# Kernel tuning notes

Hardware: AMD Instinct MI355X
Metric: run time of the kernel (lower is better)

## Reference

```python
import jax, jax.numpy as jnp
import numpy as np
import math

HEAD_DIM = 32
N_Q_HEADS = 32
N_KV_HEADS = 8
ROPE_BASE = 10000.0
NEG_INF = -1e9


def _rope_cos_sin(seq_len, dtype):
    inv_freq = 1.0 / (ROPE_BASE ** (jnp.arange(0, HEAD_DIM, 2, dtype=jnp.float32) / HEAD_DIM))
    pos = jnp.arange(seq_len, dtype=jnp.float32)
    freqs = pos[:, None] * inv_freq[None, :]          # [S, D/2]
    emb = jnp.concatenate([freqs, freqs], axis=-1)     # [S, D]
    return jnp.cos(emb).astype(dtype), jnp.sin(emb).astype(dtype)


def _rotate_half(x):
    x1, x2 = jnp.split(x, 2, axis=-1)
    return jnp.concatenate([-x2, x1], axis=-1)


def _apply_rope(x, cos, sin):
    # x: [B, H, S, D]; cos/sin: [S, D]
    return x * cos[None, None] + _rotate_half(x) * sin[None, None]


def setup_inputs() -> dict:
    key = jax.random.key(0)
    ks = jax.random.split(key, 5)
    B, S, D = 2, 2048, 1024
    sc = 1.0 / math.sqrt(D)
    return {
        "hidden_states": jax.random.normal(ks[0], (B, S, D), jnp.float32),
        "attention_mask": jnp.ones((B, S), jnp.int32),
        "Wq": jax.random.normal(ks[1], (1024, 1024), jnp.float32) * sc,
        "Wk": jax.random.normal(ks[2], (256, 1024), jnp.float32) * sc,
        "Wv": jax.random.normal(ks[3], (256, 1024), jnp.float32) * sc,
        "Wo": jax.random.normal(ks[4], (1024, 1024), jnp.float32) * sc,
    }


def reference(hidden_states, attention_mask, Wq, Wk, Wv, Wo):
    B, S, D = hidden_states.shape
    group = N_Q_HEADS // N_KV_HEADS

    q = (hidden_states @ Wq.T).reshape(B, S, N_Q_HEADS, HEAD_DIM).transpose(0, 2, 1, 3)
    k = (hidden_states @ Wk.T).reshape(B, S, N_KV_HEADS, HEAD_DIM).transpose(0, 2, 1, 3)
    v = (hidden_states @ Wv.T).reshape(B, S, N_KV_HEADS, HEAD_DIM).transpose(0, 2, 1, 3)

    cos, sin = _rope_cos_sin(S, q.dtype)
    q = _apply_rope(q, cos, sin)
    k = _apply_rope(k, cos, sin)

    k = jnp.repeat(k, group, axis=1)  # [B, 32, S, D]
    v = jnp.repeat(v, group, axis=1)

    scores = jnp.einsum("bhqd,bhkd->bhqk", q, k) / math.sqrt(HEAD_DIM)

    causal = jnp.tril(jnp.ones((S, S), bool))
    allowed = causal[None, None] & (attention_mask[:, None, None, :] != 0)
    scores = jnp.where(allowed, scores, NEG_INF)

    attn = jax.nn.softmax(scores, axis=-1)
    out = jnp.einsum("bhqk,bhkd->bhqd", attn, v)  # [B, 32, S, 32]
    out = out.transpose(0, 2, 1, 3).reshape(B, S, D)
    return out @ Wo.T
```

## Files before the change

### kernel.cpp

```cpp
#include <hip/hip_runtime.h>

typedef __bf16 bf16x8 __attribute__((ext_vector_type(8)));
typedef __bf16 bf16x4 __attribute__((ext_vector_type(4)));
typedef float f32x4 __attribute__((ext_vector_type(4)));

__device__ __forceinline__ f32x4 mfma16(bf16x8 a, bf16x8 b, f32x4 c) {
  return __builtin_amdgcn_mfma_f32_16x16x32_bf16(a, b, c, 0, 0, 0);
}

__device__ __forceinline__ float fast_exp2(float x) {
  return __builtin_amdgcn_exp2f(x);
}

__global__ __launch_bounds__(256) void prep(const float* __restrict__ hidden,
                                            const float* __restrict__ Wq,
                                            const float* __restrict__ Wk,
                                            const float* __restrict__ Wv,
                                            const float* __restrict__ Wo,
                                            __bf16* __restrict__ hb,
                                            __bf16* __restrict__ Wqkvb,
                                            __bf16* __restrict__ Wob) {
  int q = blockIdx.x * 256 + threadIdx.x;
  const float* src;
  __bf16* dst;
  if (q < 1048576) {
    src = hidden; dst = hb;
  } else if ((q -= 1048576) < 262144) {
    src = Wq; dst = Wqkvb;
  } else if ((q -= 262144) < 65536) {
    src = Wk; dst = Wqkvb + 1048576;
  } else if ((q -= 65536) < 65536) {
    src = Wv; dst = Wqkvb + 1310720;
  } else {
    q -= 65536;
    src = Wo; dst = Wob;
  }
  float4 v = *(const float4*)(src + (size_t)q * 4);
  bf16x4 o = { (__bf16)v.x, (__bf16)v.y, (__bf16)v.z, (__bf16)v.w };
  *(bf16x4*)(dst + (size_t)q * 4) = o;
}

template <bool BF16_OUT>
__global__ __launch_bounds__(256) void gemm_nt(const __bf16* __restrict__ A,
                                               const __bf16* __restrict__ B,
                                               void* __restrict__ Cv, int N) {
  __shared__ __bf16 As[2][128][32];
  __shared__ __bf16 Bs[2][128][32];
  const int m0 = blockIdx.x * 128, n0 = blockIdx.y * 128;
  const int tid = threadIdx.x;
  const int wave = tid >> 6, lane = tid & 63, quad = lane >> 4, l16 = lane & 15;
  const int wr = wave >> 1, wc = wave & 1;
  const int sr = tid >> 1, sc = (tid & 1) * 16;
  f32x4 acc[4][4] = {};
  const __bf16* Ap = A + (size_t)(m0 + sr) * 1024 + sc;
  const __bf16* Bp = B + (size_t)(n0 + sr) * 1024 + sc;
  {
    uint4 a0 = *(const uint4*)Ap, a1 = *(const uint4*)(Ap + 8);
    uint4 b0 = *(const uint4*)Bp, b1 = *(const uint4*)(Bp + 8);
    *(uint4*)&As[0][sr][sc] = a0;
    *(uint4*)&As[0][sr][sc + 8] = a1;
    *(uint4*)&Bs[0][sr][sc] = b0;
    *(uint4*)&Bs[0][sr][sc + 8] = b1;
  }
  __syncthreads();
  int buf = 0;
  for (int k0 = 0; k0 < 1024; k0 += 32) {
    const bool more = (k0 + 32) < 1024;
    uint4 na0, na1, nb0, nb1;
    if (more) {
      na0 = *(const uint4*)(Ap + k0 + 32);
      na1 = *(const uint4*)(Ap + k0 + 40);
      nb0 = *(const uint4*)(Bp + k0 + 32);
      nb1 = *(const uint4*)(Bp + k0 + 40);
    }
    bf16x8 af[4], bfr[4];
#pragma unroll
    for (int i = 0; i < 4; i++)
      af[i] = *(bf16x8*)&As[buf][64 * wr + 16 * i + l16][quad * 8];
#pragma unroll
    for (int j = 0; j < 4; j++)
      bfr[j] = *(bf16x8*)&Bs[buf][64 * wc + 16 * j + l16][quad * 8];
#pragma unroll
    for (int i = 0; i < 4; i++)
#pragma unroll
      for (int j = 0; j < 4; j++) acc[i][j] = mfma16(af[i], bfr[j], acc[i][j]);
    if (more) {
      *(uint4*)&As[buf ^ 1][sr][sc] = na0;
      *(uint4*)&As[buf ^ 1][sr][sc + 8] = na1;
      *(uint4*)&Bs[buf ^ 1][sr][sc] = nb0;
      *(uint4*)&Bs[buf ^ 1][sr][sc + 8] = nb1;
    }
    __syncthreads();
    buf ^= 1;
  }
#pragma unroll
  for (int i = 0; i < 4; i++)
#pragma unroll
    for (int j = 0; j < 4; j++)
#pragma unroll
      for (int r = 0; r < 4; r++) {
        int row = m0 + 64 * wr + 16 * i + quad * 4 + r;
        int col = n0 + 64 * wc + 16 * j + l16;
        if constexpr (BF16_OUT)
          ((__bf16*)Cv)[(size_t)row * N + col] = (__bf16)acc[i][j][r];
        else
          ((float*)Cv)[(size_t)row * N + col] = acc[i][j][r];
      }
}

__global__ __launch_bounds__(256) void ropevt(__bf16* __restrict__ QKV,
                                              __bf16* __restrict__ VT,
                                              const int* __restrict__ amask,
                                              float* __restrict__ maskb) {
  int idx = blockIdx.x * 256 + threadIdx.x;
  if (idx < 2621440) {
    __bf16* base;
    int m, i;
    if (idx < 2097152) {
      m = idx >> 9;
      int h = (idx >> 4) & 31;
      i = idx & 15;
      base = QKV + (size_t)m * 1536 + h * 32;
    } else {
      int j = idx - 2097152;
      m = j >> 7;
      int h = (j >> 4) & 7;
      i = j & 15;
      base = QKV + (size_t)m * 1536 + 1024 + h * 32;
    }
    int s = m & 2047;
    float inv = __expf(-(float)i * 0.5756462732485114f);
    float ang = (float)s * inv;
    float sn, cs;
    __sincosf(ang, &sn, &cs);
    float x0 = (float)base[i];
    float x1 = (float)base[i + 16];
    base[i] = (__bf16)(x0 * cs - x1 * sn);
    base[i + 16] = (__bf16)(x1 * cs + x0 * sn);
  } else {
    int j = idx - 2621440;
    if (j < 4096) maskb[j] = amask[j] ? -16.0f : -1.5e9f;
    int s4 = j & 511;
    int d = (j >> 9) & 31;
    int hb_ = j >> 14;
    int s = s4 * 4;
    int b_ = hb_ >> 3, hkv_ = hb_ & 7;
    const __bf16* src = QKV + (size_t)(b_ * 2048 + s) * 1536 + 1280 + hkv_ * 32 + d;
    bf16x4 ov = { src[0], src[1536], src[3072], src[4608] };
    *(bf16x4*)&VT[((size_t)hb_ * 32 + d) * 2048 + s] = ov;
  }
}

__global__ __launch_bounds__(256, 4) void attn(const __bf16* __restrict__ QKV,
                                               const __bf16* __restrict__ VT,
                                               const float* __restrict__ maskb,
                                               __bf16* __restrict__ Ob) {
  __shared__ __bf16 Ks[2][64][40];
  __shared__ __bf16 Vs[2][32][72];
  __shared__ __bf16 Pl[4][2][16][72];
  const int tid = threadIdx.x;
  const int wave = tid >> 6, lane = tid & 63;
  const int quad = lane >> 4, l16 = lane & 15;
  const int b = blockIdx.z, h = blockIdx.y, hkv = h >> 2;
  const int xp = blockIdx.x;
  const float SC2 = 0.25503472f;

  const int sk_key = tid >> 2, sk_ch = (tid & 3) * 8;
  const int sv_d = tid >> 3, sv_seg = (tid & 7) * 8;
  const __bf16* ksrc = QKV + (size_t)(b * 2048 + sk_key) * 1536 + 1024 + hkv * 32 + sk_ch;
  const __bf16* vsrc = VT + ((size_t)(b * 8 + hkv) * 32 + sv_d) * 2048 + sv_seg;
  const float* mrow = maskb + b * 2048;

  for (int sp = 0; sp < 2; sp++) {
    const int strip = sp ? 15 - xp : xp;
    const int qw = strip * 128 + wave * 32;
    const int q_row0 = qw + l16, q_row1 = qw + 16 + l16;
    const __bf16* qbase = QKV + (size_t)(b * 2048 + qw + l16) * 1536 + h * 32 + quad * 8;
    bf16x8 qf0 = *(const bf16x8*)qbase;
    bf16x8 qf1 = *(const bf16x8*)(qbase + 16 * 1536);

    {
      uint4 kr = *(const uint4*)ksrc;
      uint4 vr = *(const uint4*)vsrc;
      *(uint4*)&Ks[0][sk_key][sk_ch] = kr;
      *(uint4*)&Vs[0][sv_d][sv_seg] = vr;
    }
    __syncthreads();

    f32x4 o00 = {}, o01 = {}, o10 = {}, o11 = {};
    float rs0 = 0.f, rs1 = 0.f;
    int buf = 0;
    const int ntiles = 2 * strip + 2;

    for (int t = 0; t < ntiles; t++) {
      const int kv0 = t << 6;
      const bool more = (t + 1 < ntiles);
      uint4 kr, vr;
      if (more) {
        kr = *(const uint4*)(ksrc + (size_t)(t + 1) * 64 * 1536);
        vr = *(const uint4*)(vsrc + (size_t)(t + 1) * 64);
      }
      if (kv0 <= qw + 31) {
        bf16x8 kf[4];
#pragma unroll
        for (int kt = 0; kt < 4; kt++)
          kf[kt] = *(bf16x8*)&Ks[buf][16 * kt + l16][quad * 8];
        f32x4 s0[4], s1[4];
#pragma unroll
        for (int kt = 0; kt < 4; kt++) {
          f32x4 z = {};
          s0[kt] = mfma16(kf[kt], qf0, z);
          s1[kt] = mfma16(kf[kt], qf1, z);
        }
        float p0[4][4], p1[4][4];
        if (kv0 + 63 <= qw) {
#pragma unroll
          for (int kt = 0; kt < 4; kt++) {
            const int kb = kv0 + 16 * kt + 4 * quad;
            float4 mb = *(const float4*)(mrow + kb);
#pragma unroll
            for (int r = 0; r < 4; r++) {
              float e0 = fast_exp2(fmaf(s0[kt][r], SC2, (&mb.x)[r]));
              float e1 = fast_exp2(fmaf(s1[kt][r], SC2, (&mb.x)[r]));
              p0[kt][r] = e0;
              p1[kt][r] = e1;
              rs0 += e0;
              rs1 += e1;
            }
          }
        } else {
#pragma unroll
          for (int kt = 0; kt < 4; kt++) {
            const int kb = kv0 + 16 * kt + 4 * quad;
            float4 mb = *(const float4*)(mrow + kb);
#pragma unroll
            for (int r = 0; r < 4; r++) {
              const int key = kb + r;
              float e0 = fast_exp2(fmaf(s0[kt][r], SC2, (&mb.x)[r]));
              float e1 = fast_exp2(fmaf(s1[kt][r], SC2, (&mb.x)[r]));
              p0[kt][r] = (key <= q_row0) ? e0 : 0.f;
              p1[kt][r] = (key <= q_row1) ? e1 : 0.f;
              rs0 += p0[kt][r];
              rs1 += p1[kt][r];
            }
          }
        }
        bf16x8 vf00 = *(bf16x8*)&Vs[buf][l16][quad * 8];
        bf16x8 vf01 = *(bf16x8*)&Vs[buf][l16][32 + quad * 8];
        bf16x8 vf10 = *(bf16x8*)&Vs[buf][16 + l16][quad * 8];
        bf16x8 vf11 = *(bf16x8*)&Vs[buf][16 + l16][32 + quad * 8];
#pragma unroll
        for (int kt = 0; kt < 4; kt++) {
          bf16x4 pa = { (__bf16)p0[kt][0], (__bf16)p0[kt][1],
                        (__bf16)p0[kt][2], (__bf16)p0[kt][3] };
          bf16x4 pb = { (__bf16)p1[kt][0], (__bf16)p1[kt][1],
                        (__bf16)p1[kt][2], (__bf16)p1[kt][3] };
          *(bf16x4*)&Pl[wave][0][l16][16 * kt + 4 * quad] = pa;
          *(bf16x4*)&Pl[wave][1][l16][16 * kt + 4 * quad] = pb;
        }
        asm volatile("s_waitcnt lgkmcnt(0)" ::: "memory");
        bf16x8 pf00 = *(bf16x8*)&Pl[wave][0][l16][8 * quad];
        bf16x8 pf01 = *(bf16x8*)&Pl[wave][0][l16][32 + 8 * quad];
        bf16x8 pf10 = *(bf16x8*)&Pl[wave][1][l16][8 * quad];
        bf16x8 pf11 = *(bf16x8*)&Pl[wave][1][l16][32 + 8 * quad];
        asm volatile("s_waitcnt lgkmcnt(0)" ::: "memory");
        o00 = mfma16(vf00, pf00, o00);
        o00 = mfma16(vf01, pf01, o00);
        o01 = mfma16(vf10, pf00, o01);
        o01 = mfma16(vf11, pf01, o01);
        o10 = mfma16(vf00, pf10, o10);
        o10 = mfma16(vf01, pf11, o10);
        o11 = mfma16(vf10, pf10, o11);
        o11 = mfma16(vf11, pf11, o11);
      }
      if (more) {
        *(uint4*)&Ks[buf ^ 1][sk_key][sk_ch] = kr;
        *(uint4*)&Vs[buf ^ 1][sv_d][sv_seg] = vr;
      }
      __syncthreads();
      buf ^= 1;
    }
    rs0 += __shfl_xor(rs0, 16);
    rs0 += __shfl_xor(rs0, 32);
    rs1 += __shfl_xor(rs1, 16);
    rs1 += __shfl_xor(rs1, 32);
    float inv0 = 1.0f / rs0, inv1 = 1.0f / rs1;
    size_t row0 = (size_t)(b * 2048 + q_row0);
    size_t row1 = (size_t)(b * 2048 + q_row1);
    bf16x4 w00 = { (__bf16)(o00[0] * inv0), (__bf16)(o00[1] * inv0),
                   (__bf16)(o00[2] * inv0), (__bf16)(o00[3] * inv0) };
    bf16x4 w01 = { (__bf16)(o01[0] * inv0), (__bf16)(o01[1] * inv0),
                   (__bf16)(o01[2] * inv0), (__bf16)(o01[3] * inv0) };
    bf16x4 w10 = { (__bf16)(o10[0] * inv1), (__bf16)(o10[1] * inv1),
                   (__bf16)(o10[2] * inv1), (__bf16)(o10[3] * inv1) };
    bf16x4 w11 = { (__bf16)(o11[0] * inv1), (__bf16)(o11[1] * inv1),
                   (__bf16)(o11[2] * inv1), (__bf16)(o11[3] * inv1) };
    *(bf16x4*)&Ob[row0 * 1024 + h * 32 + quad * 4] = w00;
    *(bf16x4*)&Ob[row0 * 1024 + h * 32 + 16 + quad * 4] = w01;
    *(bf16x4*)&Ob[row1 * 1024 + h * 32 + quad * 4] = w10;
    *(bf16x4*)&Ob[row1 * 1024 + h * 32 + 16 + quad * 4] = w11;
  }
}

extern "C" void kernel_launch(void* const* d_in, const int* in_sizes, int n_in,
                              void* d_out, int out_size, void* d_ws, size_t ws_size,
                              hipStream_t stream) {
  const float* hidden = (const float*)d_in[0];
  const int* amask = (const int*)d_in[1];
  const float* Wq = (const float*)d_in[2];
  const float* Wk = (const float*)d_in[3];
  const float* Wv = (const float*)d_in[4];
  const float* Wo = (const float*)d_in[5];
  float* out = (float*)d_out;

  char* p = (char*)d_ws;
  auto carve = [&](size_t elems) {
    __bf16* r = (__bf16*)p;
    p += ((elems * 2 + 255) / 256) * 256;
    return r;
  };
  __bf16* hb = carve(4096ull * 1024);
  __bf16* Wqkvb = carve(1536ull * 1024);
  __bf16* Wob = carve(1024ull * 1024);
  __bf16* QKV = carve(4096ull * 1536);
  __bf16* VT = carve(4096ull * 256);
  __bf16* Ob = carve(4096ull * 1024);
  float* maskb = (float*)carve(8192);

  prep<<<6656, 256, 0, stream>>>(hidden, Wq, Wk, Wv, Wo, hb, Wqkvb, Wob);

  gemm_nt<true><<<dim3(32, 12), 256, 0, stream>>>(hb, Wqkvb, QKV, 1536);

  ropevt<<<11264, 256, 0, stream>>>(QKV, VT, amask, maskb);

  attn<<<dim3(8, 32, 2), 256, 0, stream>>>(QKV, VT, maskb, Ob);

  gemm_nt<false><<<dim3(32, 8), 256, 0, stream>>>(Ob, Wob, (void*)out, 1024);
}
```

Before: 195.0 us.

## Use direct global-to-LDS loads in GEMM and per-wave register K/V streaming in attention

The GEMM now stages A/B tiles with global_load_lds, which writes straight into shared memory and removes the register round trip and the explicit LDS stores. The attention kernel drops the shared K/V tiles and block-level barriers. Each wave instead independently handles a 32-row query strip and loads its K/V fragments directly from global memory into registers, double-buffered with a ping-pong lambda. This removes __syncthreads and the per-wave causal imbalance within a block, but each wave now fetches K/V itself, which raises global and L2 traffic. Occupancy is also lowered to 2 blocks per CU to fit the extra registers.

```diff
diff --git a/kernel.cpp b/kernel.cpp
--- a/kernel.cpp
+++ b/kernel.cpp
@@ -10,6 +10,12 @@
 
 __device__ __forceinline__ float fast_exp2(float x) {
   return __builtin_amdgcn_exp2f(x);
+}
+
+typedef const __attribute__((address_space(1))) void gvoid_t;
+typedef __attribute__((address_space(3))) void svoid_t;
+__device__ __forceinline__ void lds16(const __bf16* g, __bf16* l) {
+  __builtin_amdgcn_global_load_lds((gvoid_t*)g, (svoid_t*)l, 16, 0, 0);
 }
 
 __global__ __launch_bounds__(256) void prep(const float* __restrict__ hidden,
@@ -50,29 +56,22 @@
   const int tid = threadIdx.x;
   const int wave = tid >> 6, lane = tid & 63, quad = lane >> 4, l16 = lane & 15;
   const int wr = wave >> 1, wc = wave & 1;
-  const int sr = tid >> 1, sc = (tid & 1) * 16;
+  const int srow = 32 * wave;
+  const __bf16* Ag = A + (size_t)(m0 + srow + (lane >> 2)) * 1024 + (lane & 3) * 8;
+  const __bf16* Bg = B + (size_t)(n0 + srow + (lane >> 2)) * 1024 + (lane & 3) * 8;
   f32x4 acc[4][4] = {};
-  const __bf16* Ap = A + (size_t)(m0 + sr) * 1024 + sc;
-  const __bf16* Bp = B + (size_t)(n0 + sr) * 1024 + sc;
-  {
-    uint4 a0 = *(const uint4*)Ap, a1 = *(const uint4*)(Ap + 8);
-    uint4 b0 = *(const uint4*)Bp, b1 = *(const uint4*)(Bp + 8);
-    *(uint4*)&As[0][sr][sc] = a0;
-    *(uint4*)&As[0][sr][sc + 8] = a1;
-    *(uint4*)&Bs[0][sr][sc] = b0;
-    *(uint4*)&Bs[0][sr][sc + 8] = b1;
-  }
+
+  auto stage = [&](int buf, int k0) {
+    lds16(Ag + k0, &As[buf][srow][0]);
+    lds16(Ag + 16 * 1024 + k0, &As[buf][srow + 16][0]);
+    lds16(Bg + k0, &Bs[buf][srow][0]);
+    lds16(Bg + 16 * 1024 + k0, &Bs[buf][srow + 16][0]);
+  };
+  stage(0, 0);
   __syncthreads();
   int buf = 0;
   for (int k0 = 0; k0 < 1024; k0 += 32) {
-    const bool more = (k0 + 32) < 1024;
-    uint4 na0, na1, nb0, nb1;
-    if (more) {
-      na0 = *(const uint4*)(Ap + k0 + 32);
-      na1 = *(const uint4*)(Ap + k0 + 40);
-      nb0 = *(const uint4*)(Bp + k0 + 32);
-      nb1 = *(const uint4*)(Bp + k0 + 40);
-    }
+    if (k0 + 32 < 1024) stage(buf ^ 1, k0 + 32);
     bf16x8 af[4], bfr[4];
 #pragma unroll
     for (int i = 0; i < 4; i++)
@@ -84,12 +83,6 @@
     for (int i = 0; i < 4; i++)
 #pragma unroll
       for (int j = 0; j < 4; j++) acc[i][j] = mfma16(af[i], bfr[j], acc[i][j]);
-    if (more) {
-      *(uint4*)&As[buf ^ 1][sr][sc] = na0;
-      *(uint4*)&As[buf ^ 1][sr][sc + 8] = na1;
-      *(uint4*)&Bs[buf ^ 1][sr][sc] = nb0;
-      *(uint4*)&Bs[buf ^ 1][sr][sc + 8] = nb1;
-    }
     __syncthreads();
     buf ^= 1;
   }
@@ -151,135 +144,128 @@
   }
 }
 
-__global__ __launch_bounds__(256, 4) void attn(const __bf16* __restrict__ QKV,
+__global__ __launch_bounds__(256, 2) void attn(const __bf16* __restrict__ QKV,
                                                const __bf16* __restrict__ VT,
                                                const float* __restrict__ maskb,
                                                __bf16* __restrict__ Ob) {
-  __shared__ __bf16 Ks[2][64][40];
-  __shared__ __bf16 Vs[2][32][72];
   __shared__ __bf16 Pl[4][2][16][72];
   const int tid = threadIdx.x;
   const int wave = tid >> 6, lane = tid & 63;
   const int quad = lane >> 4, l16 = lane & 15;
   const int b = blockIdx.z, h = blockIdx.y, hkv = h >> 2;
-  const int xp = blockIdx.x;
+  const int xw = blockIdx.x * 4 + wave;
   const float SC2 = 0.25503472f;
-
-  const int sk_key = tid >> 2, sk_ch = (tid & 3) * 8;
-  const int sv_d = tid >> 3, sv_seg = (tid & 7) * 8;
-  const __bf16* ksrc = QKV + (size_t)(b * 2048 + sk_key) * 1536 + 1024 + hkv * 32 + sk_ch;
-  const __bf16* vsrc = VT + ((size_t)(b * 8 + hkv) * 32 + sv_d) * 2048 + sv_seg;
   const float* mrow = maskb + b * 2048;
+  const __bf16* kbase =
+      QKV + (size_t)(b * 2048 + l16) * 1536 + 1024 + hkv * 32 + quad * 8;
+  const __bf16* vbase = VT + ((size_t)(b * 8 + hkv) * 32 + l16) * 2048 + quad * 8;
 
   for (int sp = 0; sp < 2; sp++) {
-    const int strip = sp ? 15 - xp : xp;
-    const int qw = strip * 128 + wave * 32;
+    const int strip = sp ? 63 - xw : xw;
+    const int qw = strip * 32;
     const int q_row0 = qw + l16, q_row1 = qw + 16 + l16;
-    const __bf16* qbase = QKV + (size_t)(b * 2048 + qw + l16) * 1536 + h * 32 + quad * 8;
+    const __bf16* qbase =
+        QKV + (size_t)(b * 2048 + qw + l16) * 1536 + h * 32 + quad * 8;
     bf16x8 qf0 = *(const bf16x8*)qbase;
     bf16x8 qf1 = *(const bf16x8*)(qbase + 16 * 1536);
-
-    {
-      uint4 kr = *(const uint4*)ksrc;
-      uint4 vr = *(const uint4*)vsrc;
-      *(uint4*)&Ks[0][sk_key][sk_ch] = kr;
-      *(uint4*)&Vs[0][sv_d][sv_seg] = vr;
-    }
-    __syncthreads();
+    const int ntiles = ((qw + 31) >> 6) + 1;
 
     f32x4 o00 = {}, o01 = {}, o10 = {}, o11 = {};
     float rs0 = 0.f, rs1 = 0.f;
-    int buf = 0;
-    const int ntiles = 2 * strip + 2;
-
-    for (int t = 0; t < ntiles; t++) {
-      const int kv0 = t << 6;
-      const bool more = (t + 1 < ntiles);
-      uint4 kr, vr;
-      if (more) {
-        kr = *(const uint4*)(ksrc + (size_t)(t + 1) * 64 * 1536);
-        vr = *(const uint4*)(vsrc + (size_t)(t + 1) * 64);
-      }
-      if (kv0 <= qw + 31) {
-        bf16x8 kf[4];
+
+    bf16x8 kA[4], vA[4], kB[4], vB[4];
+#pragma unroll
+    for (int kt = 0; kt < 4; kt++)
+      kA[kt] = *(const bf16x8*)(kbase + (size_t)(16 * kt) * 1536);
+    vA[0] = *(const bf16x8*)(vbase);
+    vA[1] = *(const bf16x8*)(vbase + 32);
+    vA[2] = *(const bf16x8*)(vbase + 16 * 2048);
+    vA[3] = *(const bf16x8*)(vbase + 16 * 2048 + 32);
+
+    auto tile = [&](int t, bf16x8 (&kc)[4], bf16x8 (&vc)[4],
+                    bf16x8 (&kn)[4], bf16x8 (&vn)[4]) {
+      const int kv0 = t * 64;
+      if (t + 1 < ntiles) {
+        const __bf16* kp = kbase + (size_t)(kv0 + 64) * 1536;
+        const __bf16* vp = vbase + kv0 + 64;
 #pragma unroll
         for (int kt = 0; kt < 4; kt++)
-          kf[kt] = *(bf16x8*)&Ks[buf][16 * kt + l16][quad * 8];
-        f32x4 s0[4], s1[4];
+          kn[kt] = *(const bf16x8*)(kp + (size_t)(16 * kt) * 1536);
+        vn[0] = *(const bf16x8*)(vp);
+        vn[1] = *(const bf16x8*)(vp + 32);
+        vn[2] = *(const bf16x8*)(vp + 16 * 2048);
+        vn[3] = *(const bf16x8*)(vp + 16 * 2048 + 32);
+      }
+      f32x4 s0[4], s1[4];
+#pragma unroll
+      for (int kt = 0; kt < 4; kt++) {
+        f32x4 z = {};
+        s0[kt] = mfma16(kc[kt], qf0, z);
+        s1[kt] = mfma16(kc[kt], qf1, z);
+      }
+      float p0[4][4], p1[4][4];
+      if (kv0 + 63 <= qw) {
 #pragma unroll
         for (int kt = 0; kt < 4; kt++) {
-          f32x4 z = {};
-          s0[kt] = mfma16(kf[kt], qf0, z);
-          s1[kt] = mfma16(kf[kt], qf1, z);
-        }
-        float p0[4][4], p1[4][4];
-        if (kv0 + 63 <= qw) {
-#pragma unroll
-          for (int kt = 0; kt < 4; kt++) {
-            const int kb = kv0 + 16 * kt + 4 * quad;
-            float4 mb = *(const float4*)(mrow + kb);
-#pragma unroll
-            for (int r = 0; r < 4; r++) {
-              float e0 = fast_exp2(fmaf(s0[kt][r], SC2, (&mb.x)[r]));
-              float e1 = fast_exp2(fmaf(s1[kt][r], SC2, (&mb.x)[r]));
-              p0[kt][r] = e0;
-              p1[kt][r] = e1;
-              rs0 += e0;
-              rs1 += e1;
-            }
-          }
-        } else {
-#pragma unroll
-          for (int kt = 0; kt < 4; kt++) {
-            const int kb = kv0 + 16 * kt + 4 * quad;
-            float4 mb = *(const float4*)(mrow + kb);
-#pragma unroll
-            for (int r = 0; r < 4; r++) {
-              const int key = kb + r;
-              float e0 = fast_exp2(fmaf(s0[kt][r], SC2, (&mb.x)[r]));
-              float e1 = fast_exp2(fmaf(s1[kt][r], SC2, (&mb.x)[r]));
-              p0[kt][r] = (key <= q_row0) ? e0 : 0.f;
-              p1[kt][r] = (key <= q_row1) ? e1 : 0.f;
-              rs0 += p0[kt][r];
-              rs1 += p1[kt][r];
-            }
+          const int kb = kv0 + 16 * kt + 4 * quad;
+          float4 mb = *(const float4*)(mrow + kb);
+#pragma unroll
+          for (int r = 0; r < 4; r++) {
+            float e0 = fast_exp2(fmaf(s0[kt][r], SC2, (&mb.x)[r]));
+            float e1 = fast_exp2(fmaf(s1[kt][r], SC2, (&mb.x)[r]));
+            p0[kt][r] = e0;
+            p1[kt][r] = e1;
+            rs0 += e0;
+            rs1 += e1;
           }
         }
-        bf16x8 vf00 = *(bf16x8*)&Vs[buf][l16][quad * 8];
-        bf16x8 vf01 = *(bf16x8*)&Vs[buf][l16][32 + quad * 8];
-        bf16x8 vf10 = *(bf16x8*)&Vs[buf][16 + l16][quad * 8];
-        bf16x8 vf11 = *(bf16x8*)&Vs[buf][16 + l16][32 + quad * 8];
+      } else {
 #pragma unroll
         for (int kt = 0; kt < 4; kt++) {
-          bf16x4 pa = { (__bf16)p0[kt][0], (__bf16)p0[kt][1],
-                        (__bf16)p0[kt][2], (__bf16)p0[kt][3] };
-          bf16x4 pb = { (__bf16)p1[kt][0], (__bf16)p1[kt][1],
-                        (__bf16)p1[kt][2], (__bf16)p1[kt][3] };
-          *(bf16x4*)&Pl[wave][0][l16][16 * kt + 4 * quad] = pa;
-          *(bf16x4*)&Pl[wave][1][l16][16 * kt + 4 * quad] = pb;
+          const int kb = kv0 + 16 * kt + 4 * quad;
+          float4 mb = *(const float4*)(mrow + kb);
+#pragma unroll
+          for (int r = 0; r < 4; r++) {
+            const int key = kb + r;
+            float e0 = fast_exp2(fmaf(s0[kt][r], SC2, (&mb.x)[r]));
+            float e1 = fast_exp2(fmaf(s1[kt][r], SC2, (&mb.x)[r]));
+            p0[kt][r] = (key <= q_row0) ? e0 : 0.f;
+            p1[kt][r] = (key <= q_row1) ? e1 : 0.f;
+            rs0 += p0[kt][r];
+            rs1 += p1[kt][r];
+          }
         }
-        asm volatile("s_waitcnt lgkmcnt(0)" ::: "memory");
-        bf16x8 pf00 = *(bf16x8*)&Pl[wave][0][l16][8 * quad];
-        bf16x8 pf01 = *(bf16x8*)&Pl[wave][0][l16][32 + 8 * quad];
-        bf16x8 pf10 = *(bf16x8*)&Pl[wave][1][l16][8 * quad];
-        bf16x8 pf11 = *(bf16x8*)&Pl[wave][1][l16][32 + 8 * quad];
-        asm volatile("s_waitcnt lgkmcnt(0)" ::: "memory");
-        o00 = mfma16(vf00, pf00, o00);
-        o00 = mfma16(vf01, pf01, o00);
-        o01 = mfma16(vf10, pf00, o01);
-        o01 = mfma16(vf11, pf01, o01);
-        o10 = mfma16(vf00, pf10, o10);
-        o10 = mfma16(vf01, pf11, o10);
-        o11 = mfma16(vf10, pf10, o11);
-        o11 = mfma16(vf11, pf11, o11);
-      }
-      if (more) {
-        *(uint4*)&Ks[buf ^ 1][sk_key][sk_ch] = kr;
-        *(uint4*)&Vs[buf ^ 1][sv_d][sv_seg] = vr;
-      }
-      __syncthreads();
-      buf ^= 1;
+      }
+#pragma unroll
+      for (int kt = 0; kt < 4; kt++) {
+        bf16x4 pa = { (__bf16)p0[kt][0], (__bf16)p0[kt][1],
+                      (__bf16)p0[kt][2], (__bf16)p0[kt][3] };
+        bf16x4 pb = { (__bf16)p1[kt][0], (__bf16)p1[kt][1],
+                      (__bf16)p1[kt][2], (__bf16)p1[kt][3] };
+        *(bf16x4*)&Pl[wave][0][l16][16 * kt + 4 * quad] = pa;
+        *(bf16x4*)&Pl[wave][1][l16][16 * kt + 4 * quad] = pb;
+      }
+      asm volatile("s_waitcnt lgkmcnt(0)" ::: "memory");
+      bf16x8 pf00 = *(bf16x8*)&Pl[wave][0][l16][8 * quad];
+      bf16x8 pf01 = *(bf16x8*)&Pl[wave][0][l16][32 + 8 * quad];
+      bf16x8 pf10 = *(bf16x8*)&Pl[wave][1][l16][8 * quad];
+      bf16x8 pf11 = *(bf16x8*)&Pl[wave][1][l16][32 + 8 * quad];
+      asm volatile("s_waitcnt lgkmcnt(0)" ::: "memory");
+      o00 = mfma16(vc[0], pf00, o00);
+      o00 = mfma16(vc[1], pf01, o00);
+      o01 = mfma16(vc[2], pf00, o01);
+      o01 = mfma16(vc[3], pf01, o01);
+      o10 = mfma16(vc[0], pf10, o10);
+      o10 = mfma16(vc[1], pf11, o10);
+      o11 = mfma16(vc[2], pf10, o11);
+      o11 = mfma16(vc[3], pf11, o11);
+    };
+
+    for (int t = 0; t < ntiles; t += 2) {
+      tile(t, kA, vA, kB, vB);
+      if (t + 1 < ntiles) tile(t + 1, kB, vB, kA, vA);
     }
+
     rs0 += __shfl_xor(rs0, 16);
     rs0 += __shfl_xor(rs0, 32);
     rs1 += __shfl_xor(rs1, 16);
```

After: 205.3 us. 1.05x slower.
